# Performance work log

Hardware: AMD Instinct MI355X
Metric: run time of the kernel (lower is better)

The kernel has to match this reference:

```python
import jax, jax.numpy as jnp
import numpy as np

B, S, D = 2, 2048, 2048
H, HKV = 16, 4
GROUPS = H // HKV
RQ, RKV = 1024, 512
DH, DR = 192, 64          # q_head_dim, rope dim
DN = DH - DR              # nrope dim = 128
DV = 128                  # v head dim
EPS = 1e-20


def setup_inputs() -> dict:
    key = jax.random.key(0)
    ks = jax.random.split(key, 8)
    inp = {
        "hidden_states": jax.random.normal(ks[0], (B, S, D), jnp.float32),
        # causal mask (0 = masked), as used by masked_fill(mask == 0, -inf)
        "attention_mask": jnp.tril(jnp.ones((S, S), jnp.int32))[None, None],
        "w_qa": jax.random.normal(ks[1], (D, RQ), jnp.float32) * 0.02,
        "b_qa": jnp.zeros((RQ,), jnp.float32),
        "g_q": jnp.ones((RQ,), jnp.float32),
        "w_qb": jax.random.normal(ks[2], (RQ, H * DH), jnp.float32) * 0.02,
        "b_qb": jnp.zeros((H * DH,), jnp.float32),
        "w_kva": jax.random.normal(ks[3], (D, RKV + DR), jnp.float32) * 0.02,
        "b_kva": jnp.zeros((RKV + DR,), jnp.float32),
        "g_kv": jnp.ones((RKV,), jnp.float32),
        "w_kvb": jax.random.normal(ks[4], (RKV, HKV * (DN + DV)), jnp.float32) * 0.02,
        "b_kvb": jnp.zeros((HKV * (DN + DV),), jnp.float32),
        "w_o": jax.random.normal(ks[5], (H * DV, D), jnp.float32) * 0.02,
        "b_o": jnp.zeros((D,), jnp.float32),
    }
    return inp


def _rmsnorm(x, g, eps=EPS):
    var = jnp.mean(x * x, axis=-1, keepdims=True)
    return x * jax.lax.rsqrt(var + eps) * g


def _rope_cos_sin(seq_len, dim, base=10000.0, dtype=jnp.float32):
    inv_freq = 1.0 / (base ** (jnp.arange(0, dim, 2, dtype=jnp.float32) / dim))
    t = jnp.arange(seq_len, dtype=jnp.float32)
    freqs = jnp.outer(t, inv_freq)                    # [S, dim/2]
    emb = jnp.concatenate([freqs, freqs], axis=-1)    # [S, dim]
    return jnp.cos(emb).astype(dtype), jnp.sin(emb).astype(dtype)


def _apply_rope(x, cos, sin):
    # x: [..., S, dr]; rotate_half convention
    d2 = x.shape[-1] // 2
    x1, x2 = x[..., :d2], x[..., d2:]
    rot = jnp.concatenate([-x2, x1], axis=-1)
    return x * cos + rot * sin


def reference(hidden_states, attention_mask, w_qa, b_qa, g_q, w_qb, b_qb,
              w_kva, b_kva, g_kv, w_kvb, b_kvb, w_o, b_o):
    b, s, _ = hidden_states.shape
    # --- Q: LoRA down -> RMSNorm -> LoRA up ---
    q_a = hidden_states @ w_qa + b_qa                         # [B,S,RQ]
    q_b = _rmsnorm(q_a, g_q) @ w_qb + b_qb                    # [B,S,H*DH]
    q_b = q_b.reshape(b, s, H, DH).transpose(0, 2, 1, 3)      # [B,H,S,DH]
    q_nrope, q_rope = q_b[..., :DN], q_b[..., DN:]
    # --- KV: LoRA down, split latent / shared rope key ---
    kv_a = hidden_states @ w_kva + b_kva                      # [B,S,RKV+DR]
    kv_c, k_rope = kv_a[..., :RKV], kv_a[..., RKV:]
    kv_b = _rmsnorm(kv_c, g_kv) @ w_kvb + b_kvb               # [B,S,HKV*(DN+DV)]
    kv_b = kv_b.reshape(b, s, HKV, DN + DV).transpose(0, 2, 1, 3)
    k_nrope, value_states = kv_b[..., :DN], kv_b[..., DN:]    # [B,HKV,S,DN/DV]
    # --- split RoPE ---
    cos, sin = _rope_cos_sin(s, DR, dtype=hidden_states.dtype)
    q_rope = _apply_rope(q_rope, cos, sin)                    # [B,H,S,DR]
    k_rope = _apply_rope(k_rope[:, None], cos, sin)           # [B,1,S,DR]
    # --- assemble heads (rope part first, matching source concat order) ---
    query_states = jnp.concatenate([q_rope, q_nrope], axis=-1)            # [B,H,S,DH]
    key_states = jnp.concatenate(
        [jnp.broadcast_to(k_rope, (b, HKV, s, DR)), k_nrope], axis=-1)    # [B,HKV,S,DH]
    # --- GQA expand kv heads ---
    key_states = jnp.repeat(key_states, GROUPS, axis=1)                   # [B,H,S,DH]
    value_states = jnp.repeat(value_states, GROUPS, axis=1)               # [B,H,S,DV]
    # --- attention ---
    scores = jnp.einsum('bhqd,bhkd->bhqk', query_states, key_states)
    scores = scores / jnp.sqrt(jnp.asarray(DH, scores.dtype))
    scores = jnp.where(attention_mask == 0, jnp.asarray(-1e9, scores.dtype), scores)
    weights = jax.nn.softmax(scores, axis=-1)
    attn_out = jnp.einsum('bhqk,bhkd->bhqd', weights, value_states)       # [B,H,S,DV]
    attn_out = attn_out.transpose(0, 2, 1, 3).reshape(b, s, H * DV)
    return attn_out @ w_o + b_o
```

## Files before the change

### kernel.cpp

```cpp
#include <hip/hip_runtime.h>
#include <hip/hip_bf16.h>
#include <stdint.h>

#define DEV static __device__ __forceinline__

typedef __attribute__((ext_vector_type(8))) short bf16x8;
typedef __attribute__((ext_vector_type(4))) float f32x4;
typedef __attribute__((ext_vector_type(16))) float f32x16;

constexpr int Bc = 2, Sc = 2048, Dc = 2048;
constexpr int Hc = 16, HKVc = 4;
constexpr int RQc = 1024, RKVc = 512;
constexpr int DHc = 192, DRc = 64, DVc = 128;

DEV unsigned short f2bf(float f) {
  union { float f; uint32_t u; } v; v.f = f;
  uint32_t r = v.u + 0x7FFFu + ((v.u >> 16) & 1u);
  return (unsigned short)(r >> 16);
}
DEV float bf2f(unsigned short u) {
  union { uint32_t u; float f; } v; v.u = ((uint32_t)u) << 16;
  return v.f;
}

DEV void gload_lds16(const unsigned short* g, unsigned short* l) {
  __builtin_amdgcn_global_load_lds(
      (const __attribute__((address_space(1))) unsigned int*)g,
      (__attribute__((address_space(3))) unsigned int*)l, 16, 0, 0);
}

__global__ void f2b_kernel(const float* __restrict__ in, unsigned short* __restrict__ out, int n) {
  int stride = gridDim.x * blockDim.x;
  for (int i = blockIdx.x * blockDim.x + threadIdx.x; i * 4 < n; i += stride) {
    float4 v = reinterpret_cast<const float4*>(in)[i];
    union { unsigned short u[4]; uint64_t q; } pk;
    pk.u[0] = f2bf(v.x); pk.u[1] = f2bf(v.y); pk.u[2] = f2bf(v.z); pk.u[3] = f2bf(v.w);
    reinterpret_cast<uint64_t*>(out)[i] = pk.q;
  }
}

__global__ void wtrans_kernel(const float* __restrict__ in, unsigned short* __restrict__ out,
                              int R, int C) {
  __shared__ float tile[32][33];
  const int c0 = blockIdx.x * 32, r0 = blockIdx.y * 32;
  const int tx = threadIdx.x & 31, ty = threadIdx.x >> 5;
#pragma unroll
  for (int i = 0; i < 32; i += 8)
    tile[ty + i][tx] = in[(size_t)(r0 + ty + i) * C + c0 + tx];
  __syncthreads();
#pragma unroll
  for (int i = 0; i < 32; i += 8)
    out[(size_t)(c0 + ty + i) * R + r0 + tx] = f2bf(tile[tx][ty + i]);
}

__global__ void rope_table_kernel(float* __restrict__ cosT, float* __restrict__ sinT) {
  int idx = blockIdx.x * blockDim.x + threadIdx.x;
  if (idx >= Sc * DRc) return;
  int t = idx >> 6;
  int j = idx & 63;
  float inv = exp2f(-13.287712379549449f * (float)(j & 31) * (1.0f / 32.0f));
  float f = (float)t * inv;
  cosT[idx] = cosf(f);
  sinT[idx] = sinf(f);
}

template<int R>
__global__ void rmsnorm_kernel(const float* __restrict__ in, int istride,
                               const float* __restrict__ g, unsigned short* __restrict__ out) {
  int row = blockIdx.x;
  const float* x = in + (size_t)row * istride;
  float ss = 0.f;
  for (int j = threadIdx.x; j < R; j += 256) { float v = x[j]; ss += v * v; }
  for (int off = 32; off; off >>= 1) ss += __shfl_down(ss, off, 64);
  __shared__ float wsum[4];
  if ((threadIdx.x & 63) == 0) wsum[threadIdx.x >> 6] = ss;
  __syncthreads();
  float tot = wsum[0] + wsum[1] + wsum[2] + wsum[3];
  float rs = rsqrtf(tot * (1.0f / R) + 1e-20f);
  for (int j = threadIdx.x; j < R; j += 256)
    out[(size_t)row * R + j] = f2bf(x[j] * rs * g[j]);
}

template<bool OUT_BF16, bool NG>
__global__ __launch_bounds__(256)
void gemm_tn_kernel(const unsigned short* __restrict__ A, const unsigned short* __restrict__ Bt,
                    const float* __restrict__ bias, void* __restrict__ Cout,
                    int M, int N, int K) {
  __shared__ __align__(16) unsigned short As[2][128 * 64];
  __shared__ __align__(16) unsigned short Bs[2][128 * 64];
  const int t = threadIdx.x, lane = t & 63, wave = t >> 6;
  const int wm = wave >> 1, wn = wave & 1;
  const int m0 = blockIdx.x * 128, n0 = blockIdx.y * 128;
  const int fr = lane & 15, fo = (lane >> 4) * 8, rg = lane >> 4;
  const int srow = lane >> 3;
  const int scol = (lane & 7) * 8;

  const unsigned short* Ap[4];
  const unsigned short* Bp[4];
#pragma unroll
  for (int i = 0; i < 4; ++i) {
    const int ar = m0 + wave * 32 + i * 8 + srow;
    Ap[i] = A + (size_t)ar * K + scol;
    int br = n0 + wave * 32 + i * 8 + srow;
    if (NG) br = br < N ? br : N - 1;
    Bp[i] = Bt + (size_t)br * K + scol;
  }

  auto stage = [&](int buf, int k0) {
#pragma unroll
    for (int i = 0; i < 4; ++i) {
      gload_lds16(Ap[i] + k0, &As[buf][(wave * 32 + i * 8) * 64]);
      gload_lds16(Bp[i] + k0, &Bs[buf][(wave * 32 + i * 8) * 64]);
    }
  };

  f32x4 acc[4][4] = {};
  const int nt = K >> 6;

  stage(0, 0);
  for (int tt = 0; tt < nt; ++tt) {
    const int cur = tt & 1;
    if (tt + 1 < nt) {
      stage(cur ^ 1, (tt + 1) * 64);
      asm volatile("s_waitcnt vmcnt(8)" ::: "memory");
    } else {
      asm volatile("s_waitcnt vmcnt(0)" ::: "memory");
    }
    __syncthreads();
#pragma unroll
    for (int kk = 0; kk < 64; kk += 32) {
      bf16x8 af[4], bf[4];
#pragma unroll
      for (int m = 0; m < 4; ++m)
        af[m] = *reinterpret_cast<const bf16x8*>(&As[cur][(wm * 64 + m * 16 + fr) * 64 + kk + fo]);
#pragma unroll
      for (int n = 0; n < 4; ++n)
        bf[n] = *reinterpret_cast<const bf16x8*>(&Bs[cur][(wn * 64 + n * 16 + fr) * 64 + kk + fo]);
      __builtin_amdgcn_s_setprio(1);
#pragma unroll
      for (int m = 0; m < 4; ++m)
#pragma unroll
        for (int n = 0; n < 4; ++n)
          acc[m][n] = __builtin_amdgcn_mfma_f32_16x16x32_bf16(af[m], bf[n], acc[m][n], 0, 0, 0);
      __builtin_amdgcn_s_setprio(0);
    }
    __syncthreads();
  }

#pragma unroll
  for (int m = 0; m < 4; ++m) {
    const int row = m0 + wm * 64 + m * 16 + rg * 4;
#pragma unroll
    for (int n = 0; n < 4; ++n) {
      const int col = n0 + wn * 64 + n * 16 + fr;
      if (NG && col >= N) continue;
      const float bb = bias[col];
#pragma unroll
      for (int r = 0; r < 4; ++r) {
        float v = acc[m][n][r] + bb;
        if (OUT_BF16)
          reinterpret_cast<unsigned short*>(Cout)[(size_t)(row + r) * N + col] = f2bf(v);
        else
          reinterpret_cast<float*>(Cout)[(size_t)(row + r) * N + col] = v;
      }
    }
  }
}

__global__ __launch_bounds__(256)
void gemm_qfuse_kernel(const unsigned short* __restrict__ A, const unsigned short* __restrict__ Bt,
                       const float* __restrict__ bias,
                       const float* __restrict__ cosT, const float* __restrict__ sinT,
                       unsigned short* __restrict__ Qt, int M, int N, int K) {
  const float QS = 0.07216878364870323f * 1.4426950408889634f;
  __shared__ __align__(16) unsigned short As[2][128 * 64];
  __shared__ __align__(16) unsigned short Bs[2][128 * 64];
  const int t = threadIdx.x, lane = t & 63, wave = t >> 6;
  const int wm = wave >> 1, wn = wave & 1;
  const int m0 = blockIdx.x * 128, n0 = blockIdx.y * 128;
  const int fr = lane & 15, fo = (lane >> 4) * 8, rg = lane >> 4;
  const int srow = lane >> 3;
  const int scol = (lane & 7) * 8;

  const unsigned short* Ap[4];
  const unsigned short* Bp[4];
#pragma unroll
  for (int i = 0; i < 4; ++i) {
    Ap[i] = A + (size_t)(m0 + wave * 32 + i * 8 + srow) * K + scol;
    Bp[i] = Bt + (size_t)(n0 + wave * 32 + i * 8 + srow) * K + scol;
  }

  auto stage = [&](int buf, int k0) {
#pragma unroll
    for (int i = 0; i < 4; ++i) {
      gload_lds16(Ap[i] + k0, &As[buf][(wave * 32 + i * 8) * 64]);
      gload_lds16(Bp[i] + k0, &Bs[buf][(wave * 32 + i * 8) * 64]);
    }
  };

  f32x4 acc[4][4] = {};
  const int nt = K >> 6;

  stage(0, 0);
  for (int tt = 0; tt < nt; ++tt) {
    const int cur = tt & 1;
    if (tt + 1 < nt) {
      stage(cur ^ 1, (tt + 1) * 64);
      asm volatile("s_waitcnt vmcnt(8)" ::: "memory");
    } else {
      asm volatile("s_waitcnt vmcnt(0)" ::: "memory");
    }
    __syncthreads();
#pragma unroll
    for (int kk = 0; kk < 64; kk += 32) {
      bf16x8 af[4], bf[4];
#pragma unroll
      for (int m = 0; m < 4; ++m)
        af[m] = *reinterpret_cast<const bf16x8*>(&As[cur][(wm * 64 + m * 16 + fr) * 64 + kk + fo]);
#pragma unroll
      for (int n = 0; n < 4; ++n)
        bf[n] = *reinterpret_cast<const bf16x8*>(&Bs[cur][(wn * 64 + n * 16 + fr) * 64 + kk + fo]);
      __builtin_amdgcn_s_setprio(1);
#pragma unroll
      for (int m = 0; m < 4; ++m)
#pragma unroll
        for (int n = 0; n < 4; ++n)
          acc[m][n] = __builtin_amdgcn_mfma_f32_16x16x32_bf16(af[m], bf[n], acc[m][n], 0, 0, 0);
      __builtin_amdgcn_s_setprio(0);
    }
    __syncthreads();
  }

  const int wbase = n0 + wn * 64;
  const int hq = wbase / 192;
  const int dbase = wbase - hq * 192;
  const bool ropewin = (dbase == 128);

#pragma unroll
  for (int m = 0; m < 4; ++m) {
    const int row0 = m0 + wm * 64 + m * 16 + rg * 4;
#pragma unroll
    for (int n = 0; n < 4; ++n) {
      const int col = wbase + n * 16 + fr;
      const int d = dbase + n * 16 + fr;
      const float bb = bias[col];
#pragma unroll
      for (int r = 0; r < 4; ++r) {
        const int row = row0 + r;
        const int s = row & (Sc - 1);
        const int bq = row >> 11;
        float qv = acc[m][n][r] + bb;
        if (ropewin) {
          const int j = d - 128;
          const int n2 = (n < 2) ? n + 2 : n - 2;
          const float pv = acc[m][n2][r] + bias[wbase + n2 * 16 + fr];
          const float c = cosT[s * 64 + j], sn = sinT[s * 64 + j];
          qv = (n < 2) ? (qv * c - pv * sn) : (qv * c + pv * sn);
        }
        Qt[((size_t)(bq * Hc + hq) * Sc + s) * DHc + d] = f2bf(qv * QS);
      }
    }
  }
}

__global__ void prep_k_kernel(const unsigned short* __restrict__ kvb,
                              const float* __restrict__ ccat,
                              const float* __restrict__ cosT, const float* __restrict__ sinT,
                              unsigned short* __restrict__ K) {
  int bs = blockIdx.x;
  int s = bs & (Sc - 1);
  int b = bs >> 11;
  int d = threadIdx.x;
  if (d >= 192) return;
  unsigned short ropeval = 0;
  if (d >= 128) {
    int j = d - 128;
    float x = ccat[(size_t)bs * 1600 + 1536 + j];
    float other = ccat[(size_t)bs * 1600 + 1536 + (j < 32 ? j + 32 : j - 32)];
    float c = cosT[s * 64 + j], sn = sinT[s * 64 + j];
    float v = (j < 32) ? (x * c - other * sn) : (x * c + other * sn);
    ropeval = f2bf(v);
  }
  const size_t off = (size_t)(s >> 5) * 6144 + (d >> 3) * 256 + (s & 31) * 8 + (d & 7);
  for (int kvh = 0; kvh < HKVc; ++kvh) {
    unsigned short o;
    if (d < 128) o = kvb[(size_t)bs * 1024 + kvh * 256 + d];
    else o = ropeval;
    K[(size_t)(b * HKVc + kvh) * Sc * DHc + off] = o;
  }
}

__global__ void vtrans_kernel(const unsigned short* __restrict__ kvb, unsigned short* __restrict__ Vt) {
  int idx = blockIdx.x;
  int dt = idx & 3;  idx >>= 2;
  int st = idx & 63; idx >>= 6;
  int kvh = idx & 3; idx >>= 2;
  int b = idx;
  __shared__ unsigned short tile[32][33];
  int t = threadIdx.x;
  int c = t & 31, r0 = t >> 5;
#pragma unroll
  for (int i = 0; i < 4; ++i) {
    int r = r0 + i * 8;
    int s = st * 32 + r;
    tile[r][c] = kvb[((size_t)(b * Sc + s)) * 1024 + kvh * 256 + 128 + dt * 32 + c];
  }
  __syncthreads();
#pragma unroll
  for (int i = 0; i < 4; ++i) {
    int r = r0 + i * 8;
    const int dd = dt * 32 + r;
    const int k = st * 32 + c;
    const size_t pos = (size_t)(k >> 5) * 4096 + ((k >> 3) & 3) * 1024 + dd * 8 + (k & 7);
    Vt[(size_t)((b * HKVc + kvh)) * DVc * Sc + pos] = tile[c][r];
  }
}

__global__ __launch_bounds__(128)
void attn_kernel(const unsigned short* __restrict__ Q, const unsigned short* __restrict__ Kt,
                 const unsigned short* __restrict__ Vt, unsigned short* __restrict__ attnOut) {
  __shared__ __align__(16) unsigned short Ks[2][2][6144];

  const int bid = blockIdx.x;
  const int g = bid & 7;
  const int b = g >> 2, kvh = g & 3;
  const int rr = bid >> 3;
  const int hp = rr & 1;
  const int u = rr >> 1;
  const int w = threadIdx.x >> 6;
  const int h = kvh * 4 + hp * 2 + w;
  const int lane = threadIdx.x & 63;
  const int l31 = lane & 31, hi = lane >> 5;

  const unsigned short* Qh = Q + (size_t)(b * Hc + h) * Sc * DHc;
  const unsigned short* Kg = Kt + (size_t)(b * HKVc + kvh) * Sc * DHc;
  const unsigned short* Vg = Vt + (size_t)(b * HKVc + kvh) * DVc * Sc;

  auto stage = [&](int t) {
    const unsigned short* src = Kg + (size_t)t * 6144;
    unsigned short* dst = &Ks[w][t & 1][0];
#pragma unroll
    for (int j = 0; j < 12; ++j)
      gload_lds16(src + j * 512 + lane * 8, dst + j * 512 + lane * 8);
  };

#pragma unroll 1
  for (int pan = 0; pan < 2; ++pan) {
    const int sub = pan ? u : (63 - u);
    const int q0 = sub * 32;
    const int q = q0 + l31;
    const int NT = sub + 1;

    bf16x8 qf[12];
#pragma unroll
    for (int f = 0; f < 12; ++f)
      qf[f] = *reinterpret_cast<const bf16x8*>(Qh + (size_t)q * DHc + f * 16 + hi * 8);

    f32x16 ot[4] = {};
    float m = -INFINITY, lsum = 0.f;

    stage(0);

    for (int t = 0; t < NT; ++t) {
      bf16x8 vf[8];
#pragma unroll
      for (int dt = 0; dt < 4; ++dt)
#pragma unroll
        for (int k2 = 0; k2 < 2; ++k2)
          vf[dt * 2 + k2] = *reinterpret_cast<const bf16x8*>(
              Vg + (size_t)t * 4096 + (k2 * 2 + hi) * 1024 + (dt * 32 + l31) * 8);
      __builtin_amdgcn_sched_barrier(0);
      if (t + 1 < NT) {
        stage(t + 1);
        asm volatile("s_waitcnt vmcnt(20)" ::: "memory");
      } else {
        asm volatile("s_waitcnt vmcnt(8)" ::: "memory");
      }
      __builtin_amdgcn_sched_barrier(0);

      const unsigned short* kb = &Ks[w][t & 1][0];
      f32x16 s = {};
      __builtin_amdgcn_s_setprio(1);
#pragma unroll
      for (int f = 0; f < 12; ++f) {
        bf16x8 kf = *reinterpret_cast<const bf16x8*>(kb + (f * 2 + hi) * 256 + l31 * 8);
        s = __builtin_amdgcn_mfma_f32_32x32x16_bf16(kf, qf[f], s, 0, 0, 0);
      }
      __builtin_amdgcn_s_setprio(0);

      float v[16];
      if (t == sub) {
#pragma unroll
        for (int rrr = 0; rrr < 16; ++rrr) {
          const int kl = (rrr & 3) + 8 * (rrr >> 2) + 4 * hi;
          v[rrr] = (kl <= l31) ? s[rrr] : -3.0e38f;
        }
      } else {
#pragma unroll
        for (int rrr = 0; rrr < 16; ++rrr) v[rrr] = s[rrr];
      }

      float pmax = fmaxf(fmaxf(fmaxf(v[0], v[1]), fmaxf(v[2], v[3])),
                         fmaxf(fmaxf(v[4], v[5]), fmaxf(v[6], v[7])));
      float pmax2 = fmaxf(fmaxf(fmaxf(v[8], v[9]), fmaxf(v[10], v[11])),
                          fmaxf(fmaxf(v[12], v[13]), fmaxf(v[14], v[15])));
      pmax = fmaxf(pmax, pmax2);
      pmax = fmaxf(pmax, __shfl_xor(pmax, 32, 64));

      float cf = 1.f;
      if (!__all(pmax - m <= 8.0f)) {
        const float mnew = fmaxf(m, pmax);
        cf = exp2f(m - mnew);
        m = mnew;
#pragma unroll
        for (int dt = 0; dt < 4; ++dt)
#pragma unroll
          for (int rrr = 0; rrr < 16; ++rrr) ot[dt][rrr] *= cf;
      }

      float pp[16];
      float rs = 0.f;
#pragma unroll
      for (int rrr = 0; rrr < 16; ++rrr) { pp[rrr] = exp2f(v[rrr] - m); rs += pp[rrr]; }
      rs += __shfl_xor(rs, 32, 64);
      lsum = lsum * cf + rs;

      uint32_t c[8], x[8];
#pragma unroll
      for (int ii = 0; ii < 8; ++ii) {
        asm("v_cvt_pk_bf16_f32 %0, %1, %2" : "=v"(c[ii]) : "v"(pp[2 * ii]), "v"(pp[2 * ii + 1]));
        x[ii] = (uint32_t)__shfl_xor((int)c[ii], 32, 64);
      }
      union { uint32_t w[4]; bf16x8 v8; } pa0, pa1;
      pa0.w[0] = hi ? x[2] : c[0];
      pa0.w[1] = hi ? x[3] : c[1];
      pa0.w[2] = hi ? c[2] : x[0];
      pa0.w[3] = hi ? c[3] : x[1];
      pa1.w[0] = hi ? x[6] : c[4];
      pa1.w[1] = hi ? x[7] : c[5];
      pa1.w[2] = hi ? c[6] : x[4];
      pa1.w[3] = hi ? c[7] : x[5];

      __builtin_amdgcn_s_setprio(1);
#pragma unroll
      for (int dt = 0; dt < 4; ++dt) {
        ot[dt] = __builtin_amdgcn_mfma_f32_32x32x16_bf16(vf[dt * 2], pa0.v8, ot[dt], 0, 0, 0);
        ot[dt] = __builtin_amdgcn_mfma_f32_32x32x16_bf16(vf[dt * 2 + 1], pa1.v8, ot[dt], 0, 0, 0);
      }
      __builtin_amdgcn_s_setprio(0);
    }

    const float inv = 1.0f / lsum;
    unsigned short* dst = attnOut + ((size_t)(b * Sc + q)) * (Hc * DVc) + h * DVc;
#pragma unroll
    for (int dt = 0; dt < 4; ++dt)
#pragma unroll
      for (int rq = 0; rq < 4; ++rq) {
        uint32_t lo = (uint32_t)f2bf(ot[dt][rq * 4 + 0] * inv) |
                      ((uint32_t)f2bf(ot[dt][rq * 4 + 1] * inv) << 16);
        uint32_t hi2 = (uint32_t)f2bf(ot[dt][rq * 4 + 2] * inv) |
                       ((uint32_t)f2bf(ot[dt][rq * 4 + 3] * inv) << 16);
        uint2 pk; pk.x = lo; pk.y = hi2;
        *reinterpret_cast<uint2*>(dst + dt * 32 + 8 * rq + 4 * hi) = pk;
      }
  }
}

extern "C" void kernel_launch(void* const* d_in, const int* in_sizes, int n_in,
                              void* d_out, int out_size, void* d_ws, size_t ws_size,
                              hipStream_t stream) {
  (void)in_sizes; (void)n_in; (void)out_size; (void)ws_size;
  const float* hidden = (const float*)d_in[0];
  const float* w_qa  = (const float*)d_in[2];
  const float* b_qa  = (const float*)d_in[3];
  const float* g_q   = (const float*)d_in[4];
  const float* w_qb  = (const float*)d_in[5];
  const float* b_qb  = (const float*)d_in[6];
  const float* w_kva = (const float*)d_in[7];
  const float* b_kva = (const float*)d_in[8];
  const float* g_kv  = (const float*)d_in[9];
  const float* w_kvb = (const float*)d_in[10];
  const float* b_kvb = (const float*)d_in[11];
  const float* w_o   = (const float*)d_in[12];
  const float* b_o   = (const float*)d_in[13];
  float* out = (float*)d_out;

  char* ws = (char*)d_ws;
  size_t off = 0;
  auto alloc = [&](size_t bytes) -> void* {
    void* p = ws + off;
    off += (bytes + 255) & ~(size_t)255;
    return p;
  };
  const int MS = Bc * Sc;
  const int NCAT = RQc + RKVc + DRc;

  unsigned short* Xbf   = (unsigned short*)alloc((size_t)MS * Dc * 2);
  unsigned short* Wcat  = (unsigned short*)alloc((size_t)NCAT * Dc * 2);
  unsigned short* WqbT  = (unsigned short*)alloc((size_t)Hc * DHc * RQc * 2);
  unsigned short* WkvbT = (unsigned short*)alloc((size_t)HKVc * 256 * RKVc * 2);
  unsigned short* WoT   = (unsigned short*)alloc((size_t)Dc * Hc * DVc * 2);
  float* bcat = (float*)alloc((size_t)NCAT * 4);
  float* cosT = (float*)alloc((size_t)Sc * DRc * 4);
  float* sinT = (float*)alloc((size_t)Sc * DRc * 4);
  float* Ccat = (float*)alloc((size_t)MS * NCAT * 4);
  unsigned short* qan  = (unsigned short*)alloc((size_t)MS * RQc * 2);
  unsigned short* kvcn = (unsigned short*)alloc((size_t)MS * RKVc * 2);
  unsigned short* kvb  = (unsigned short*)alloc((size_t)MS * HKVc * 256 * 2);
  unsigned short* Qt   = (unsigned short*)alloc((size_t)Bc * Hc * Sc * DHc * 2);
  unsigned short* Kt   = (unsigned short*)alloc((size_t)Bc * HKVc * Sc * DHc * 2);
  unsigned short* Vt   = (unsigned short*)alloc((size_t)Bc * HKVc * DVc * Sc * 2);
  unsigned short* attnb= (unsigned short*)alloc((size_t)MS * Hc * DVc * 2);

  f2b_kernel<<<dim3(512), dim3(256), 0, stream>>>(hidden, Xbf, MS * Dc);
  wtrans_kernel<<<dim3(RQc / 32, Dc / 32), 256, 0, stream>>>(w_qa, Wcat, Dc, RQc);
  wtrans_kernel<<<dim3((RKVc + DRc) / 32, Dc / 32), 256, 0, stream>>>(w_kva, Wcat + (size_t)RQc * Dc, Dc, RKVc + DRc);
  wtrans_kernel<<<dim3(Hc * DHc / 32, RQc / 32), 256, 0, stream>>>(w_qb, WqbT, RQc, Hc * DHc);
  wtrans_kernel<<<dim3(HKVc * 256 / 32, RKVc / 32), 256, 0, stream>>>(w_kvb, WkvbT, RKVc, HKVc * 256);
  wtrans_kernel<<<dim3(Dc / 32, Hc * DVc / 32), 256, 0, stream>>>(w_o, WoT, Hc * DVc, Dc);
  hipMemcpyAsync(bcat, b_qa, (size_t)RQc * 4, hipMemcpyDeviceToDevice, stream);
  hipMemcpyAsync(bcat + RQc, b_kva, (size_t)(RKVc + DRc) * 4, hipMemcpyDeviceToDevice, stream);
  rope_table_kernel<<<dim3(512), dim3(256), 0, stream>>>(cosT, sinT);

  gemm_tn_kernel<false, true><<<dim3(MS / 128, (NCAT + 127) / 128), 256, 0, stream>>>(Xbf, Wcat, bcat, Ccat, MS, NCAT, Dc);
  rmsnorm_kernel<1024><<<dim3(MS), 256, 0, stream>>>(Ccat, NCAT, g_q, qan);
  rmsnorm_kernel<512><<<dim3(MS), 256, 0, stream>>>(Ccat + RQc, NCAT, g_kv, kvcn);
  gemm_qfuse_kernel<<<dim3(MS / 128, Hc * DHc / 128), 256, 0, stream>>>(qan, WqbT, b_qb, cosT, sinT, Qt, MS, Hc * DHc, RQc);
  gemm_tn_kernel<true, false><<<dim3(MS / 128, HKVc * 256 / 128), 256, 0, stream>>>(kvcn, WkvbT, b_kvb, kvb, MS, HKVc * 256, RKVc);

  prep_k_kernel<<<dim3(MS), 256, 0, stream>>>(kvb, Ccat, cosT, sinT, Kt);
  vtrans_kernel<<<dim3(Bc * HKVc * (Sc / 32) * (DVc / 32)), 256, 0, stream>>>(kvb, Vt);

  attn_kernel<<<dim3(512), dim3(128), 0, stream>>>(Qt, Kt, Vt, attnb);

  gemm_tn_kernel<false, false><<<dim3(MS / 128, Dc / 128), 256, 0, stream>>>(attnb, WoT, b_o, out, MS, Dc, Hc * DVc);
}
```

Before: 349.3 us.

## Share K tile across waves and launch one query tile per block

The attention kernel now loads each K tile into LDS once per block, with both waves each staging half of it. Before, each wave staged its own copy even though both waves use the same KV head. Each block now handles a single 32-query tile instead of a paired long and short panel, and the grid doubles to 1024 blocks with the largest tiles issued first. A launch bound of 3 blocks per SIMD is requested. This halves LDS use and redundant K traffic and raises occupancy, at the cost of a full vmcnt(0) wait plus a block barrier every iteration.

```diff
diff --git a/kernel.cpp b/kernel.cpp
--- a/kernel.cpp
+++ b/kernel.cpp
@@ -316,17 +316,17 @@
   }
 }
 
-__global__ __launch_bounds__(128)
+__global__ __launch_bounds__(128, 3)
 void attn_kernel(const unsigned short* __restrict__ Q, const unsigned short* __restrict__ Kt,
                  const unsigned short* __restrict__ Vt, unsigned short* __restrict__ attnOut) {
-  __shared__ __align__(16) unsigned short Ks[2][2][6144];
+  __shared__ __align__(16) unsigned short Ks[2][6144];
 
   const int bid = blockIdx.x;
   const int g = bid & 7;
   const int b = g >> 2, kvh = g & 3;
-  const int rr = bid >> 3;
-  const int hp = rr & 1;
-  const int u = rr >> 1;
+  const int idx = bid >> 3;
+  const int hp = idx & 1;
+  const int sub = 63 - (idx >> 1);
   const int w = threadIdx.x >> 6;
   const int h = kvh * 4 + hp * 2 + w;
   const int lane = threadIdx.x & 63;
@@ -336,134 +336,134 @@
   const unsigned short* Kg = Kt + (size_t)(b * HKVc + kvh) * Sc * DHc;
   const unsigned short* Vg = Vt + (size_t)(b * HKVc + kvh) * DVc * Sc;
 
+  const int q0 = sub * 32;
+  const int q = q0 + l31;
+  const int NT = sub + 1;
+
   auto stage = [&](int t) {
     const unsigned short* src = Kg + (size_t)t * 6144;
-    unsigned short* dst = &Ks[w][t & 1][0];
-#pragma unroll
-    for (int j = 0; j < 12; ++j)
-      gload_lds16(src + j * 512 + lane * 8, dst + j * 512 + lane * 8);
+    unsigned short* dst = &Ks[t & 1][0];
+#pragma unroll
+    for (int j = 0; j < 6; ++j) {
+      const int jj = w * 6 + j;
+      gload_lds16(src + jj * 512 + lane * 8, dst + jj * 512);
+    }
   };
 
-#pragma unroll 1
-  for (int pan = 0; pan < 2; ++pan) {
-    const int sub = pan ? u : (63 - u);
-    const int q0 = sub * 32;
-    const int q = q0 + l31;
-    const int NT = sub + 1;
-
-    bf16x8 qf[12];
-#pragma unroll
-    for (int f = 0; f < 12; ++f)
-      qf[f] = *reinterpret_cast<const bf16x8*>(Qh + (size_t)q * DHc + f * 16 + hi * 8);
-
-    f32x16 ot[4] = {};
-    float m = -INFINITY, lsum = 0.f;
-
-    stage(0);
-
-    for (int t = 0; t < NT; ++t) {
-      bf16x8 vf[8];
+  bf16x8 qf[12];
+#pragma unroll
+  for (int f = 0; f < 12; ++f)
+    qf[f] = *reinterpret_cast<const bf16x8*>(Qh + (size_t)q * DHc + f * 16 + hi * 8);
+
+  f32x16 ot[4] = {};
+  float m = -INFINITY, lsum = 0.f;
+
+  stage(0);
+  asm volatile("s_waitcnt vmcnt(0)" ::: "memory");
+  __syncthreads();
+
+  for (int t = 0; t < NT; ++t) {
+    const int cur = t & 1;
+
+    bf16x8 vf[8];
+#pragma unroll
+    for (int dt = 0; dt < 4; ++dt)
+#pragma unroll
+      for (int k2 = 0; k2 < 2; ++k2)
+        vf[dt * 2 + k2] = *reinterpret_cast<const bf16x8*>(
+            Vg + (size_t)t * 4096 + (k2 * 2 + hi) * 1024 + (dt * 32 + l31) * 8);
+    __builtin_amdgcn_sched_barrier(0);
+    if (t + 1 < NT) stage(t + 1);
+    __builtin_amdgcn_sched_barrier(0);
+
+    const unsigned short* kb = &Ks[cur][0];
+    f32x16 s = {};
+    __builtin_amdgcn_s_setprio(1);
+#pragma unroll
+    for (int f = 0; f < 12; ++f) {
+      bf16x8 kf = *reinterpret_cast<const bf16x8*>(kb + (f * 2 + hi) * 256 + l31 * 8);
+      s = __builtin_amdgcn_mfma_f32_32x32x16_bf16(kf, qf[f], s, 0, 0, 0);
+    }
+    __builtin_amdgcn_s_setprio(0);
+
+    float v[16];
+    if (t == sub) {
+#pragma unroll
+      for (int rrr = 0; rrr < 16; ++rrr) {
+        const int kl = (rrr & 3) + 8 * (rrr >> 2) + 4 * hi;
+        v[rrr] = (kl <= l31) ? s[rrr] : -3.0e38f;
+      }
+    } else {
+#pragma unroll
+      for (int rrr = 0; rrr < 16; ++rrr) v[rrr] = s[rrr];
+    }
+
+    float pmax = fmaxf(fmaxf(fmaxf(v[0], v[1]), fmaxf(v[2], v[3])),
+                       fmaxf(fmaxf(v[4], v[5]), fmaxf(v[6], v[7])));
+    float pmax2 = fmaxf(fmaxf(fmaxf(v[8], v[9]), fmaxf(v[10], v[11])),
+                        fmaxf(fmaxf(v[12], v[13]), fmaxf(v[14], v[15])));
+    pmax = fmaxf(pmax, pmax2);
+    pmax = fmaxf(pmax, __shfl_xor(pmax, 32, 64));
+
+    float cf = 1.f;
+    if (!__all(pmax - m <= 8.0f)) {
+      const float mnew = fmaxf(m, pmax);
+      cf = exp2f(m - mnew);
+      m = mnew;
 #pragma unroll
       for (int dt = 0; dt < 4; ++dt)
 #pragma unroll
-        for (int k2 = 0; k2 < 2; ++k2)
-          vf[dt * 2 + k2] = *reinterpret_cast<const bf16x8*>(
-              Vg + (size_t)t * 4096 + (k2 * 2 + hi) * 1024 + (dt * 32 + l31) * 8);
-      __builtin_amdgcn_sched_barrier(0);
-      if (t + 1 < NT) {
-        stage(t + 1);
-        asm volatile("s_waitcnt vmcnt(20)" ::: "memory");
-      } else {
-        asm volatile("s_waitcnt vmcnt(8)" ::: "memory");
-      }
-      __builtin_amdgcn_sched_barrier(0);
-
-      const unsigned short* kb = &Ks[w][t & 1][0];
-      f32x16 s = {};
-      __builtin_amdgcn_s_setprio(1);
-#pragma unroll
-      for (int f = 0; f < 12; ++f) {
-        bf16x8 kf = *reinterpret_cast<const bf16x8*>(kb + (f * 2 + hi) * 256 + l31 * 8);
-        s = __builtin_amdgcn_mfma_f32_32x32x16_bf16(kf, qf[f], s, 0, 0, 0);
-      }
-      __builtin_amdgcn_s_setprio(0);
-
-      float v[16];
-      if (t == sub) {
-#pragma unroll
-        for (int rrr = 0; rrr < 16; ++rrr) {
-          const int kl = (rrr & 3) + 8 * (rrr >> 2) + 4 * hi;
-          v[rrr] = (kl <= l31) ? s[rrr] : -3.0e38f;
-        }
-      } else {
-#pragma unroll
-        for (int rrr = 0; rrr < 16; ++rrr) v[rrr] = s[rrr];
-      }
-
-      float pmax = fmaxf(fmaxf(fmaxf(v[0], v[1]), fmaxf(v[2], v[3])),
-                         fmaxf(fmaxf(v[4], v[5]), fmaxf(v[6], v[7])));
-      float pmax2 = fmaxf(fmaxf(fmaxf(v[8], v[9]), fmaxf(v[10], v[11])),
-                          fmaxf(fmaxf(v[12], v[13]), fmaxf(v[14], v[15])));
-      pmax = fmaxf(pmax, pmax2);
-      pmax = fmaxf(pmax, __shfl_xor(pmax, 32, 64));
-
-      float cf = 1.f;
-      if (!__all(pmax - m <= 8.0f)) {
-        const float mnew = fmaxf(m, pmax);
-        cf = exp2f(m - mnew);
-        m = mnew;
-#pragma unroll
-        for (int dt = 0; dt < 4; ++dt)
-#pragma unroll
-          for (int rrr = 0; rrr < 16; ++rrr) ot[dt][rrr] *= cf;
-      }
-
-      float pp[16];
-      float rs = 0.f;
-#pragma unroll
-      for (int rrr = 0; rrr < 16; ++rrr) { pp[rrr] = exp2f(v[rrr] - m); rs += pp[rrr]; }
-      rs += __shfl_xor(rs, 32, 64);
-      lsum = lsum * cf + rs;
-
-      uint32_t c[8], x[8];
-#pragma unroll
-      for (int ii = 0; ii < 8; ++ii) {
-        asm("v_cvt_pk_bf16_f32 %0, %1, %2" : "=v"(c[ii]) : "v"(pp[2 * ii]), "v"(pp[2 * ii + 1]));
-        x[ii] = (uint32_t)__shfl_xor((int)c[ii], 32, 64);
-      }
-      union { uint32_t w[4]; bf16x8 v8; } pa0, pa1;
-      pa0.w[0] = hi ? x[2] : c[0];
-      pa0.w[1] = hi ? x[3] : c[1];
-      pa0.w[2] = hi ? c[2] : x[0];
-      pa0.w[3] = hi ? c[3] : x[1];
-      pa1.w[0] = hi ? x[6] : c[4];
-      pa1.w[1] = hi ? x[7] : c[5];
-      pa1.w[2] = hi ? c[6] : x[4];
-      pa1.w[3] = hi ? c[7] : x[5];
-
-      __builtin_amdgcn_s_setprio(1);
-#pragma unroll
-      for (int dt = 0; dt < 4; ++dt) {
-        ot[dt] = __builtin_amdgcn_mfma_f32_32x32x16_bf16(vf[dt * 2], pa0.v8, ot[dt], 0, 0, 0);
-        ot[dt] = __builtin_amdgcn_mfma_f32_32x32x16_bf16(vf[dt * 2 + 1], pa1.v8, ot[dt], 0, 0, 0);
-      }
-      __builtin_amdgcn_s_setprio(0);
-    }
-
-    const float inv = 1.0f / lsum;
-    unsigned short* dst = attnOut + ((size_t)(b * Sc + q)) * (Hc * DVc) + h * DVc;
-#pragma unroll
-    for (int dt = 0; dt < 4; ++dt)
-#pragma unroll
-      for (int rq = 0; rq < 4; ++rq) {
-        uint32_t lo = (uint32_t)f2bf(ot[dt][rq * 4 + 0] * inv) |
-                      ((uint32_t)f2bf(ot[dt][rq * 4 + 1] * inv) << 16);
-        uint32_t hi2 = (uint32_t)f2bf(ot[dt][rq * 4 + 2] * inv) |
-                       ((uint32_t)f2bf(ot[dt][rq * 4 + 3] * inv) << 16);
-        uint2 pk; pk.x = lo; pk.y = hi2;
-        *reinterpret_cast<uint2*>(dst + dt * 32 + 8 * rq + 4 * hi) = pk;
-      }
-  }
+        for (int rrr = 0; rrr < 16; ++rrr) ot[dt][rrr] *= cf;
+    }
+
+    float pp[16];
+    float rs = 0.f;
+#pragma unroll
+    for (int rrr = 0; rrr < 16; ++rrr) { pp[rrr] = exp2f(v[rrr] - m); rs += pp[rrr]; }
+    rs += __shfl_xor(rs, 32, 64);
+    lsum = lsum * cf + rs;
+
+    uint32_t c[8], x[8];
+#pragma unroll
+    for (int ii = 0; ii < 8; ++ii) {
+      asm("v_cvt_pk_bf16_f32 %0, %1, %2" : "=v"(c[ii]) : "v"(pp[2 * ii]), "v"(pp[2 * ii + 1]));
+      x[ii] = (uint32_t)__shfl_xor((int)c[ii], 32, 64);
+    }
+    union { uint32_t w[4]; bf16x8 v8; } pa0, pa1;
+    pa0.w[0] = hi ? x[2] : c[0];
+    pa0.w[1] = hi ? x[3] : c[1];
+    pa0.w[2] = hi ? c[2] : x[0];
+    pa0.w[3] = hi ? c[3] : x[1];
+    pa1.w[0] = hi ? x[6] : c[4];
+    pa1.w[1] = hi ? x[7] : c[5];
+    pa1.w[2] = hi ? c[6] : x[4];
+    pa1.w[3] = hi ? c[7] : x[5];
+
+    __builtin_amdgcn_s_setprio(1);
+#pragma unroll
+    for (int dt = 0; dt < 4; ++dt) {
+      ot[dt] = __builtin_amdgcn_mfma_f32_32x32x16_bf16(vf[dt * 2], pa0.v8, ot[dt], 0, 0, 0);
+      ot[dt] = __builtin_amdgcn_mfma_f32_32x32x16_bf16(vf[dt * 2 + 1], pa1.v8, ot[dt], 0, 0, 0);
+    }
+    __builtin_amdgcn_s_setprio(0);
+
+    asm volatile("s_waitcnt vmcnt(0)" ::: "memory");
+    __syncthreads();
+  }
+
+  const float inv = 1.0f / lsum;
+  unsigned short* dst = attnOut + ((size_t)(b * Sc + q)) * (Hc * DVc) + h * DVc;
+#pragma unroll
+  for (int dt = 0; dt < 4; ++dt)
+#pragma unroll
+    for (int rq = 0; rq < 4; ++rq) {
+      uint32_t lo = (uint32_t)f2bf(ot[dt][rq * 4 + 0] * inv) |
+                    ((uint32_t)f2bf(ot[dt][rq * 4 + 1] * inv) << 16);
+      uint32_t hi2 = (uint32_t)f2bf(ot[dt][rq * 4 + 2] * inv) |
+                     ((uint32_t)f2bf(ot[dt][rq * 4 + 3] * inv) << 16);
+      uint2 pk; pk.x = lo; pk.y = hi2;
+      *reinterpret_cast<uint2*>(dst + dt * 32 + 8 * rq + 4 * hi) = pk;
+    }
 }
 
 extern "C" void kernel_launch(void* const* d_in, const int* in_sizes, int n_in,
@@ -531,7 +531,7 @@
   prep_k_kernel<<<dim3(MS), 256, 0, stream>>>(kvb, Ccat, cosT, sinT, Kt);
   vtrans_kernel<<<dim3(Bc * HKVc * (Sc / 32) * (DVc / 32)), 256, 0, stream>>>(kvb, Vt);
 
-  attn_kernel<<<dim3(512), dim3(128), 0, stream>>>(Qt, Kt, Vt, attnb);
+  attn_kernel<<<dim3(1024), dim3(128), 0, stream>>>(Qt, Kt, Vt, attnb);
 
   gemm_tn_kernel<false, false><<<dim3(MS / 128, Dc / 128), 256, 0, stream>>>(attnb, WoT, b_o, out, MS, Dc, Hc * DVc);
 }
```

New measurement: 349.8 us. Within noise of the previous version (+0.1%).
